# Performance work log

Measured on AMD Instinct MI355X. Metric: run time of the kernel, lower is better.

## Reference

```python
import jax, jax.numpy as jnp
import numpy as np

TAU = 0.2
EPS = 1e-12  # torch F.normalize eps

def _l2norm(x):
    n = jnp.sqrt(jnp.sum(x * x, axis=-1, keepdims=True))
    return x / jnp.maximum(n, EPS)

def setup_inputs() -> dict:
    key = jax.random.key(0)
    k1, k2 = jax.random.split(key)
    B, Nx, Ny, D = 2, 8192, 8192, 128
    feat_x = jax.random.normal(k1, (B, Nx, D), dtype=jnp.float32)
    feat_y = jax.random.normal(k2, (B, Ny, D), dtype=jnp.float32)
    verts_mask_x = jnp.ones((B, Nx), dtype=jnp.float32)
    verts_mask_y = jnp.ones((B, Ny), dtype=jnp.float32)
    return {"feat_x": feat_x, "feat_y": feat_y, "verts_mask_x": verts_mask_x, "verts_mask_y": verts_mask_y}

def reference(feat_x, feat_y, verts_mask_x, verts_mask_y):
    # cosine similarity scores: [B, Nx, Ny]
    log_alpha = jnp.einsum('bxd,byd->bxy', _l2norm(feat_x), _l2norm(feat_y)) / TAU
    # stable softmax over last dim (normalise_dim = -1)
    alpha = jax.nn.softmax(log_alpha, axis=-1)
    # double masking: rows by mask_x, cols by mask_y
    return alpha * verts_mask_x[:, :, None] * verts_mask_y[:, None, :]
```

## Files before the change

### kernel.cpp

```cpp
#include <hip/hip_runtime.h>
#include <hip/hip_bf16.h>


typedef __attribute__((ext_vector_type(8))) short short8;
typedef __attribute__((ext_vector_type(4))) float float4v;

constexpr int B = 2, NX = 8192, NY = 8192, DD = 128;
constexpr int BM = 128, BN = 128;
constexpr int NSPLIT = 8;
constexpr int YCHUNK = NY / NSPLIT;
constexpr int LDP = 136;
constexpr float TAU_INV = 5.0f;

__global__ __launch_bounds__(256) void l2norm_kernel(const float* __restrict__ in,
                                                     __hip_bfloat16* __restrict__ out,
                                                     int rows) {
    int wid = threadIdx.x >> 6, lane = threadIdx.x & 63;
    int row = blockIdx.x * 4 + wid;
    if (row >= rows) return;
    float2 v = ((const float2*)(in + (size_t)row * DD))[lane];
    float ss = v.x * v.x + v.y * v.y;
#pragma unroll
    for (int off = 32; off >= 1; off >>= 1) ss += __shfl_xor(ss, off);
    float inv = 1.0f / fmaxf(sqrtf(ss), 1e-12f);
    __hip_bfloat162 o;
    o.x = __float2bfloat16(v.x * inv);
    o.y = __float2bfloat16(v.y * inv);
    ((__hip_bfloat162*)(out + (size_t)row * DD))[lane] = o;
}

__global__ __launch_bounds__(256) void pass1_kernel(const __hip_bfloat16* __restrict__ Xn,
                                                    const __hip_bfloat16* __restrict__ Yn,
                                                    float* __restrict__ partial) {
    __shared__ __hip_bfloat16 Xs[BM][LDP];
    __shared__ __hip_bfloat16 Ys[BN][LDP];
    const int split = blockIdx.x, xt = blockIdx.y, b = blockIdx.z;
    const int t = threadIdx.x;
    const int lane = t & 63, wid = t >> 6;
    const int wm = wid >> 1, wn = wid & 1;
    const int lrow = lane & 15, lhi = lane >> 4;

    {
        const __hip_bfloat16* gx = Xn + (size_t)(b * NX + xt * BM) * DD;
#pragma unroll
        for (int i = 0; i < 8; ++i) {
            int r = i * 16 + (t >> 4);
            int c = (t & 15) * 8;
            *(int4*)(&Xs[r][c]) = *(const int4*)(gx + (size_t)r * DD + c);
        }
    }

    float run[4][4];
#pragma unroll
    for (int m = 0; m < 4; ++m)
#pragma unroll
        for (int r = 0; r < 4; ++r) run[m][r] = 0.f;

    for (int tile = 0; tile < YCHUNK / BN; ++tile) {
        __syncthreads();
        const __hip_bfloat16* gy = Yn + (size_t)(b * NY + split * YCHUNK + tile * BN) * DD;
#pragma unroll
        for (int i = 0; i < 8; ++i) {
            int r = i * 16 + (t >> 4);
            int c = (t & 15) * 8;
            *(int4*)(&Ys[r][c]) = *(const int4*)(gy + (size_t)r * DD + c);
        }
        __syncthreads();

        float4v acc[4][4];
#pragma unroll
        for (int m = 0; m < 4; ++m)
#pragma unroll
            for (int n = 0; n < 4; ++n) acc[m][n] = (float4v)(0.f);
#pragma unroll
        for (int kk = 0; kk < 4; ++kk) {
            short8 a[4], bb[4];
#pragma unroll
            for (int m = 0; m < 4; ++m)
                a[m] = *(const short8*)(&Xs[wm * 64 + m * 16 + lrow][kk * 32 + lhi * 8]);
#pragma unroll
            for (int n = 0; n < 4; ++n)
                bb[n] = *(const short8*)(&Ys[wn * 64 + n * 16 + lrow][kk * 32 + lhi * 8]);
#pragma unroll
            for (int m = 0; m < 4; ++m)
#pragma unroll
                for (int n = 0; n < 4; ++n)
                    acc[m][n] = __builtin_amdgcn_mfma_f32_16x16x32_bf16(a[m], bb[n], acc[m][n], 0, 0, 0);
        }
#pragma unroll
        for (int m = 0; m < 4; ++m)
#pragma unroll
            for (int r = 0; r < 4; ++r) {
                float s = 0.f;
#pragma unroll
                for (int n = 0; n < 4; ++n) s += __expf(acc[m][n][r] * TAU_INV);
                run[m][r] += s;
            }
    }

#pragma unroll
    for (int m = 0; m < 4; ++m)
#pragma unroll
        for (int r = 0; r < 4; ++r) {
            float v = run[m][r];
            v += __shfl_xor(v, 1);
            v += __shfl_xor(v, 2);
            v += __shfl_xor(v, 4);
            v += __shfl_xor(v, 8);
            run[m][r] = v;
        }

    __syncthreads();
    float* lred = (float*)Ys;
    if (lrow == 0) {
#pragma unroll
        for (int m = 0; m < 4; ++m)
#pragma unroll
            for (int r = 0; r < 4; ++r) {
                int xl = wm * 64 + m * 16 + lhi * 4 + r;
                lred[wn * BM + xl] = run[m][r];
            }
    }
    __syncthreads();
    if (t < BM) {
        float tot = lred[t] + lred[BM + t];
        partial[(size_t)split * (B * NX) + (size_t)b * NX + xt * BM + t] = tot;
    }
}

__global__ void combine_kernel(const float* __restrict__ partial,
                               const float* __restrict__ maskx,
                               float* __restrict__ rowscale) {
    int idx = blockIdx.x * 256 + threadIdx.x;
    if (idx >= B * NX) return;
    float s = 0.f;
#pragma unroll
    for (int i = 0; i < NSPLIT; ++i) s += partial[(size_t)i * (B * NX) + idx];
    rowscale[idx] = maskx[idx] / s;
}

__global__ __launch_bounds__(256) void pass2_kernel(const __hip_bfloat16* __restrict__ Xn,
                                                    const __hip_bfloat16* __restrict__ Yn,
                                                    const float* __restrict__ rowscale,
                                                    const float* __restrict__ masky,
                                                    float* __restrict__ out) {
    __shared__ __hip_bfloat16 Xs[BM][LDP];
    __shared__ __hip_bfloat16 Ys[BN][LDP];
    const int yt = blockIdx.x, xt = blockIdx.y, b = blockIdx.z;
    const int t = threadIdx.x;
    const int lane = t & 63, wid = t >> 6;
    const int wm = wid >> 1, wn = wid & 1;
    const int lrow = lane & 15, lhi = lane >> 4;

    {
        const __hip_bfloat16* gx = Xn + (size_t)(b * NX + xt * BM) * DD;
        const __hip_bfloat16* gy = Yn + (size_t)(b * NY + yt * BN) * DD;
#pragma unroll
        for (int i = 0; i < 8; ++i) {
            int r = i * 16 + (t >> 4);
            int c = (t & 15) * 8;
            *(int4*)(&Xs[r][c]) = *(const int4*)(gx + (size_t)r * DD + c);
            *(int4*)(&Ys[r][c]) = *(const int4*)(gy + (size_t)r * DD + c);
        }
    }
    __syncthreads();

    float4v acc[4][4];
#pragma unroll
    for (int m = 0; m < 4; ++m)
#pragma unroll
        for (int n = 0; n < 4; ++n) acc[m][n] = (float4v)(0.f);
#pragma unroll
    for (int kk = 0; kk < 4; ++kk) {
        short8 a[4], bb[4];
#pragma unroll
        for (int m = 0; m < 4; ++m)
            a[m] = *(const short8*)(&Xs[wm * 64 + m * 16 + lrow][kk * 32 + lhi * 8]);
#pragma unroll
        for (int n = 0; n < 4; ++n)
            bb[n] = *(const short8*)(&Ys[wn * 64 + n * 16 + lrow][kk * 32 + lhi * 8]);
#pragma unroll
        for (int m = 0; m < 4; ++m)
#pragma unroll
            for (int n = 0; n < 4; ++n)
                acc[m][n] = __builtin_amdgcn_mfma_f32_16x16x32_bf16(a[m], bb[n], acc[m][n], 0, 0, 0);
    }

    float my[4];
#pragma unroll
    for (int n = 0; n < 4; ++n)
        my[n] = masky[(size_t)b * NY + yt * BN + wn * 64 + n * 16 + lrow];

#pragma unroll
    for (int m = 0; m < 4; ++m) {
        const int xbase = xt * BM + wm * 64 + m * 16 + lhi * 4;
#pragma unroll
        for (int r = 0; r < 4; ++r) {
            const int x = xbase + r;
            const float rs = rowscale[(size_t)b * NX + x];
            float* orow = out + ((size_t)b * NX + x) * NY + yt * BN + wn * 64 + lrow;
#pragma unroll
            for (int n = 0; n < 4; ++n)
                orow[n * 16] = __expf(acc[m][n][r] * TAU_INV) * rs * my[n];
        }
    }
}

extern "C" void kernel_launch(void* const* d_in, const int* in_sizes, int n_in,
                              void* d_out, int out_size, void* d_ws, size_t ws_size,
                              hipStream_t stream) {
    const float* feat_x = (const float*)d_in[0];
    const float* feat_y = (const float*)d_in[1];
    const float* maskx  = (const float*)d_in[2];
    const float* masky  = (const float*)d_in[3];
    float* out = (float*)d_out;

    char* ws = (char*)d_ws;
    __hip_bfloat16* Xn = (__hip_bfloat16*)ws;
    __hip_bfloat16* Yn = (__hip_bfloat16*)(ws + (size_t)B * NX * DD * 2);
    float* partial  = (float*)(ws + (size_t)B * (NX + NY) * DD * 2);
    float* rowscale = partial + (size_t)NSPLIT * B * NX;

    l2norm_kernel<<<B * NX / 4, 256, 0, stream>>>(feat_x, Xn, B * NX);
    l2norm_kernel<<<B * NY / 4, 256, 0, stream>>>(feat_y, Yn, B * NY);
    pass1_kernel<<<dim3(NSPLIT, NX / BM, B), 256, 0, stream>>>(Xn, Yn, partial);
    combine_kernel<<<(B * NX + 255) / 256, 256, 0, stream>>>(partial, maskx, rowscale);
    pass2_kernel<<<dim3(NY / BN, NX / BM, B), 256, 0, stream>>>(Xn, Yn, rowscale, masky, out);
}
```

Before: 180.4 us.

## Swap MFMA operands in pass2 for vectorized nontemporal float4 output stores

Pass2 now places Y rows in the A operand and X rows in the B operand. Each lane's four accumulator values then lie along contiguous y columns of one output row, so the output can be written as float4 stores instead of scattered scalar stores. Those stores use nontemporal hints to avoid polluting the cache with the 512MB output. The LDS staging and __syncthreads are removed, and fragments are loaded directly from global memory (L2-resident bf16), which could add global load latency and redundant reads.

```diff
diff --git a/kernel.cpp b/kernel.cpp
--- a/kernel.cpp
+++ b/kernel.cpp
@@ -144,64 +144,60 @@
                                                     const float* __restrict__ rowscale,
                                                     const float* __restrict__ masky,
                                                     float* __restrict__ out) {
-    __shared__ __hip_bfloat16 Xs[BM][LDP];
-    __shared__ __hip_bfloat16 Ys[BN][LDP];
     const int yt = blockIdx.x, xt = blockIdx.y, b = blockIdx.z;
     const int t = threadIdx.x;
     const int lane = t & 63, wid = t >> 6;
-    const int wm = wid >> 1, wn = wid & 1;
+    const int wy = wid >> 1, wx = wid & 1;
     const int lrow = lane & 15, lhi = lane >> 4;
 
-    {
-        const __hip_bfloat16* gx = Xn + (size_t)(b * NX + xt * BM) * DD;
-        const __hip_bfloat16* gy = Yn + (size_t)(b * NY + yt * BN) * DD;
-#pragma unroll
-        for (int i = 0; i < 8; ++i) {
-            int r = i * 16 + (t >> 4);
-            int c = (t & 15) * 8;
-            *(int4*)(&Xs[r][c]) = *(const int4*)(gx + (size_t)r * DD + c);
-            *(int4*)(&Ys[r][c]) = *(const int4*)(gy + (size_t)r * DD + c);
-        }
-    }
-    __syncthreads();
+    const int ybase = yt * BN + wy * 64;
+    const int xbase = xt * BM + wx * 64;
+
+    const __hip_bfloat16* gy = Yn + (size_t)(b * NY + ybase + lrow) * DD + lhi * 8;
+    const __hip_bfloat16* gx = Xn + (size_t)(b * NX + xbase + lrow) * DD + lhi * 8;
 
     float4v acc[4][4];
 #pragma unroll
-    for (int m = 0; m < 4; ++m)
-#pragma unroll
-        for (int n = 0; n < 4; ++n) acc[m][n] = (float4v)(0.f);
+    for (int n = 0; n < 4; ++n)
+#pragma unroll
+        for (int m = 0; m < 4; ++m) acc[n][m] = (float4v)(0.f);
+
 #pragma unroll
     for (int kk = 0; kk < 4; ++kk) {
         short8 a[4], bb[4];
 #pragma unroll
-        for (int m = 0; m < 4; ++m)
-            a[m] = *(const short8*)(&Xs[wm * 64 + m * 16 + lrow][kk * 32 + lhi * 8]);
-#pragma unroll
         for (int n = 0; n < 4; ++n)
-            bb[n] = *(const short8*)(&Ys[wn * 64 + n * 16 + lrow][kk * 32 + lhi * 8]);
-#pragma unroll
-        for (int m = 0; m < 4; ++m)
-#pragma unroll
-            for (int n = 0; n < 4; ++n)
-                acc[m][n] = __builtin_amdgcn_mfma_f32_16x16x32_bf16(a[m], bb[n], acc[m][n], 0, 0, 0);
-    }
-
-    float my[4];
+            a[n] = *(const short8*)(gy + (size_t)(n * 16) * DD + kk * 32);
+#pragma unroll
+        for (int m = 0; m < 4; ++m)
+            bb[m] = *(const short8*)(gx + (size_t)(m * 16) * DD + kk * 32);
+#pragma unroll
+        for (int n = 0; n < 4; ++n)
+#pragma unroll
+            for (int m = 0; m < 4; ++m)
+                acc[n][m] = __builtin_amdgcn_mfma_f32_16x16x32_bf16(a[n], bb[m], acc[n][m], 0, 0, 0);
+    }
+
+    float rs[4];
+#pragma unroll
+    for (int m = 0; m < 4; ++m)
+        rs[m] = rowscale[(size_t)b * NX + xbase + m * 16 + lrow];
+    float4v my4[4];
 #pragma unroll
     for (int n = 0; n < 4; ++n)
-        my[n] = masky[(size_t)b * NY + yt * BN + wn * 64 + n * 16 + lrow];
+        my4[n] = *(const float4v*)(masky + (size_t)b * NY + ybase + n * 16 + lhi * 4);
 
 #pragma unroll
     for (int m = 0; m < 4; ++m) {
-        const int xbase = xt * BM + wm * 64 + m * 16 + lhi * 4;
-#pragma unroll
-        for (int r = 0; r < 4; ++r) {
-            const int x = xbase + r;
-            const float rs = rowscale[(size_t)b * NX + x];
-            float* orow = out + ((size_t)b * NX + x) * NY + yt * BN + wn * 64 + lrow;
-#pragma unroll
-            for (int n = 0; n < 4; ++n)
-                orow[n * 16] = __expf(acc[m][n][r] * TAU_INV) * rs * my[n];
+        const int x = xbase + m * 16 + lrow;
+        float* orow = out + ((size_t)b * NX + x) * NY;
+#pragma unroll
+        for (int n = 0; n < 4; ++n) {
+            float4v o;
+#pragma unroll
+            for (int r = 0; r < 4; ++r)
+                o[r] = __expf(acc[n][m][r] * TAU_INV) * rs[m] * my4[n][r];
+            __builtin_nontemporal_store(o, (float4v*)(orow + ybase + n * 16 + lhi * 4));
         }
     }
 }
```

After: 224.4 us. 24.4% more time.
